# Kernel optimization log

Hardware: AMD Instinct MI355X
Metric: run time of the kernel (lower is better)

Reference implementation:

```python
import jax, jax.numpy as jnp
import numpy as np

B, S, D, H = 4, 2048, 512, 8
DEPTH = D // H


def setup_inputs() -> dict:
    key = jax.random.key(0)
    ks = jax.random.split(key, 12)
    s = 0.02
    return {
        "q": jax.random.normal(ks[0], (B, S, D), jnp.float32),
        "k": jax.random.normal(ks[1], (B, S, D), jnp.float32),
        "v": jax.random.normal(ks[2], (B, S, D), jnp.float32),
        "mask": jax.random.randint(ks[3], (B, 1, 1, S), 0, 2, jnp.int32),
        "wq": jax.random.normal(ks[4], (D, D), jnp.float32) * s,
        "bq": jnp.zeros((D,), jnp.float32),
        "wk": jax.random.normal(ks[5], (D, D), jnp.float32) * s,
        "bk": jnp.zeros((D,), jnp.float32),
        "wv": jax.random.normal(ks[6], (D, D), jnp.float32) * s,
        "bv": jnp.zeros((D,), jnp.float32),
        "wo": jax.random.normal(ks[7], (D, D), jnp.float32) * s,
        "bo": jnp.zeros((D,), jnp.float32),
    }


def _split_heads(x):
    # [B,S,D] -> [B,H,S,depth]
    b = x.shape[0]
    return x.reshape(b, -1, H, DEPTH).transpose(0, 2, 1, 3)


def reference(q, k, v, mask, wq, bq, wk, bk, wv, bv, wo, bo):
    qh = _split_heads(q @ wq + bq)
    kh = _split_heads(k @ wk + bk)
    vh = _split_heads(v @ wv + bv)
    scale = 1.0 / jnp.sqrt(jnp.float32(DEPTH))
    logits = jnp.einsum("bhqd,bhkd->bhqk", qh, kh) * scale
    logits = logits + mask.astype(jnp.float32) * -1e9
    attn = jax.nn.softmax(logits, axis=-1)  # [B,H,Sq,Sk]
    out = jnp.einsum("bhqk,bhkd->bhqd", attn, vh)
    out = out.transpose(0, 2, 1, 3).reshape(q.shape[0], -1, D)
    out = out @ wo + bo
    return out, attn
```

## Files before the change

### kernel.cpp

```cpp
#include <hip/hip_runtime.h>

#define B_ 4
#define S_ 2048
#define D_ 512
#define H_ 8
#define DP_ 64
#define NT_ (S_/64)

typedef __attribute__((ext_vector_type(4))) float f32x4;
typedef __attribute__((ext_vector_type(8))) short short8;
typedef __attribute__((ext_vector_type(4))) int i32x4;

__device__ __forceinline__ short f2bf(float f){
  unsigned u = __float_as_uint(f);
  u += 0x7fff + ((u >> 16) & 1);
  return (short)(u >> 16);
}

__device__ __forceinline__ int cvtpk(float lo, float hi){
  int r;
  asm("v_cvt_pk_bf16_f32 %0, %1, %2" : "=v"(r) : "v"(lo), "v"(hi));
  return r;
}

#define SWZ(r, kb) ((r)*64 + ((kb) ^ (((r)&7)<<3)))
#define F2(r) ((((r)&3)) | ((((r)>>3)&1)<<2))
#define SWZ2(r, kb) ((r)*64 + ((kb) ^ (F2(r)<<3)))

#define WAITV(N) do{ asm volatile("s_waitcnt vmcnt(" #N ")" ::: "memory"); }while(0)
#define BAR() do{ __builtin_amdgcn_s_barrier(); __builtin_amdgcn_sched_barrier(0); }while(0)

template<int NC>
__device__ __forceinline__ void stage_swz(const short* __restrict__ g, int rowStride,
                                          short* shbase, int w, int l){
  #pragma unroll
  for(int i = 0; i < NC; ++i){
    int byte = (w*NC + i)*1024 + l*16;
    int row = byte >> 7;
    int gs = ((byte >> 4) & 7) ^ (row & 7);
    const short* src = g + (size_t)row*rowStride + gs*8;
    __builtin_amdgcn_global_load_lds((const __attribute__((address_space(1))) void*)src,
        (__attribute__((address_space(3))) void*)(shbase + (w*NC + i)*512), 16, 0, 0);
  }
}
template<int NC>
__device__ __forceinline__ void stage_swz2(const short* __restrict__ g, int rowStride,
                                           short* shbase, int w, int l){
  #pragma unroll
  for(int i = 0; i < NC; ++i){
    int byte = (w*NC + i)*1024 + l*16;
    int row = byte >> 7;
    int gs = ((byte >> 4) & 7) ^ F2(row);
    const short* src = g + (size_t)row*rowStride + gs*8;
    __builtin_amdgcn_global_load_lds((const __attribute__((address_space(1))) void*)src,
        (__attribute__((address_space(3))) void*)(shbase + (w*NC + i)*512), 16, 0, 0);
  }
}

__global__ __launch_bounds__(256) void k_pre(const float* __restrict__ q,
        const float* __restrict__ k, const float* __restrict__ v,
        const int* __restrict__ mask,
        const float* __restrict__ w0, const float* __restrict__ w1,
        const float* __restrict__ w2, const float* __restrict__ w3,
        short* __restrict__ wT, short* __restrict__ qkvc, float* __restrict__ mb){
  __shared__ float tt[32][33];
  const int bi = blockIdx.x, t = threadIdx.x;
  if(bi < 1024){
    const int z = bi >> 8;
    const float* w = z == 0 ? w0 : z == 1 ? w1 : z == 2 ? w2 : w3;
    short* wt = wT + z * 262144;
    const int bxy = bi & 255;
    const int bx = (bxy & 15) * 32, by = (bxy >> 4) * 32;
    const int tx = t & 31, ty = t >> 5;
    #pragma unroll
    for(int i = 0; i < 32; i += 8) tt[ty + i][tx] = w[(by + ty + i) * D_ + bx + tx];
    __syncthreads();
    #pragma unroll
    for(int i = 0; i < 32; i += 8) wt[(bx + ty + i) * D_ + by + tx] = f2bf(tt[tx][ty + i]);
  } else if(bi < 7168){
    const int ci = bi - 1024;
    const int z = ci >> 11;
    const float* s = z == 0 ? q : z == 1 ? k : v;
    short* d = qkvc + (size_t)z * (B_ * S_ * D_);
    int i = (ci & 2047) * 256 + t;
    float4 a = ((const float4*)s)[i * 2];
    float4 b = ((const float4*)s)[i * 2 + 1];
    short8 o;
    o[0]=f2bf(a.x); o[1]=f2bf(a.y); o[2]=f2bf(a.z); o[3]=f2bf(a.w);
    o[4]=f2bf(b.x); o[5]=f2bf(b.y); o[6]=f2bf(b.z); o[7]=f2bf(b.w);
    ((short8*)d)[i] = o;
  } else {
    int i = (bi - 7168) * 256 + t;
    mb[i] = mask[i] ? -1.0e9f : 0.0f;
  }
}

__global__ __launch_bounds__(256) void k_gemm_qkv(const short* __restrict__ Xall,
        const short* __restrict__ WTall, const float* __restrict__ b0,
        const float* __restrict__ b1, const float* __restrict__ b2,
        short* __restrict__ qh, short* __restrict__ kh, short* __restrict__ vvt){
  __shared__ __align__(16) short As[8192];
  __shared__ __align__(16) short Bs[8192];
  const int z = blockIdx.z;
  const short* X  = Xall + (size_t)z * (B_*S_*D_);
  const short* WT = WTall + (size_t)z * (D_*D_);
  const float* bias = z==0 ? b0 : (z==1 ? b1 : b2);
  const int t = threadIdx.x, l = t & 63, w = t >> 6;
  const int lr = l & 15, lg = l >> 4;
  const int m0 = blockIdx.x * 128, n0 = blockIdx.y * 128;
  const int wr = w >> 1, wc = w & 1;
  const short* Xb = X + (size_t)m0 * D_;
  const short* Wb = WT + (size_t)n0 * D_;
  f32x4 acc[4][4] = {};
  for(int kt = 0; kt < D_ / 64; ++kt){
    stage_swz<4>(Xb + kt*64, D_, As, w, l);
    stage_swz<4>(Wb + kt*64, D_, Bs, w, l);
    __syncthreads();
    #pragma unroll
    for(int ks = 0; ks < 2; ++ks){
      const int kb = ks*32 + lg*8;
      short8 a[4], b[4];
      #pragma unroll
      for(int mt = 0; mt < 4; ++mt)
        a[mt] = *reinterpret_cast<const short8*>(&As[SWZ(wr*64 + mt*16 + lr, kb)]);
      #pragma unroll
      for(int nt = 0; nt < 4; ++nt)
        b[nt] = *reinterpret_cast<const short8*>(&Bs[SWZ(wc*64 + nt*16 + lr, kb)]);
      __builtin_amdgcn_s_setprio(1);
      #pragma unroll
      for(int mt = 0; mt < 4; ++mt)
        #pragma unroll
        for(int nt = 0; nt < 4; ++nt)
          acc[mt][nt] = __builtin_amdgcn_mfma_f32_16x16x32_bf16(a[mt], b[nt], acc[mt][nt], 0, 0, 0);
      __builtin_amdgcn_s_setprio(0);
    }
    __syncthreads();
  }
  #pragma unroll
  for(int mt = 0; mt < 4; ++mt){
    #pragma unroll
    for(int nt = 0; nt < 4; ++nt){
      const int n = n0 + wc*64 + nt*16 + lr;
      const int m4 = m0 + wr*64 + mt*16 + lg*4;
      float vals[4];
      #pragma unroll
      for(int r = 0; r < 4; ++r) vals[r] = acc[mt][nt][r] + bias[n];
      if(z == 2){
        short4 pv4;
        pv4.x = f2bf(vals[0]); pv4.y = f2bf(vals[1]); pv4.z = f2bf(vals[2]); pv4.w = f2bf(vals[3]);
        *reinterpret_cast<short4*>(&vvt[
            (((size_t)((m4 >> 11) * H_ + (n >> 6))) * DP_ + (n & 63)) * S_ + (m4 & 2047)]) = pv4;
      } else {
        short* dst = z == 0 ? qh : kh;
        #pragma unroll
        for(int r = 0; r < 4; ++r){
          int m = m4 + r;
          dst[(((size_t)((m >> 11) * H_ + (n >> 6))) * S_ + (m & 2047)) * DP_ + (n & 63)] = f2bf(vals[r]);
        }
      }
    }
  }
}

__global__ __launch_bounds__(256) void k_gemm_out(const short* __restrict__ X,
        const short* __restrict__ WT, const float* __restrict__ bias,
        float* __restrict__ Out){
  __shared__ __align__(16) short As[8192];
  __shared__ __align__(16) short Bs[8192];
  const int t = threadIdx.x, l = t & 63, w = t >> 6;
  const int lr = l & 15, lg = l >> 4;
  const int m0 = blockIdx.x * 128, n0 = blockIdx.y * 128;
  const int wr = w >> 1, wc = w & 1;
  const short* Xb = X + (size_t)m0 * D_;
  const short* Wb = WT + (size_t)n0 * D_;
  f32x4 acc[4][4] = {};
  for(int kt = 0; kt < D_ / 64; ++kt){
    stage_swz<4>(Xb + kt*64, D_, As, w, l);
    stage_swz<4>(Wb + kt*64, D_, Bs, w, l);
    __syncthreads();
    #pragma unroll
    for(int ks = 0; ks < 2; ++ks){
      const int kb = ks*32 + lg*8;
      short8 a[4], b[4];
      #pragma unroll
      for(int mt = 0; mt < 4; ++mt)
        a[mt] = *reinterpret_cast<const short8*>(&As[SWZ(wr*64 + mt*16 + lr, kb)]);
      #pragma unroll
      for(int nt = 0; nt < 4; ++nt)
        b[nt] = *reinterpret_cast<const short8*>(&Bs[SWZ(wc*64 + nt*16 + lr, kb)]);
      __builtin_amdgcn_s_setprio(1);
      #pragma unroll
      for(int mt = 0; mt < 4; ++mt)
        #pragma unroll
        for(int nt = 0; nt < 4; ++nt)
          acc[mt][nt] = __builtin_amdgcn_mfma_f32_16x16x32_bf16(a[mt], b[nt], acc[mt][nt], 0, 0, 0);
      __builtin_amdgcn_s_setprio(0);
    }
    __syncthreads();
  }
  #pragma unroll
  for(int mt = 0; mt < 4; ++mt){
    #pragma unroll
    for(int nt = 0; nt < 4; ++nt){
      const int n = n0 + wc*64 + nt*16 + lr;
      const int m4 = m0 + wr*64 + mt*16 + lg*4;
      #pragma unroll
      for(int r = 0; r < 4; ++r)
        Out[(size_t)(m4 + r) * D_ + n] = acc[mt][nt][r] + bias[n];
    }
  }
}

__global__ __launch_bounds__(512, 4) void k_attn(const short* __restrict__ qh,
                                                 const short* __restrict__ kh,
                                                 const short* __restrict__ vt,
                                                 const float* __restrict__ mb,
                                                 float* __restrict__ attn,
                                                 short* __restrict__ ctx){
  __shared__ __align__(16) short Sh[28672];
  const int t = threadIdx.x, l = t & 63, w = t >> 6;
  const int lr = l & 15, lg = l >> 4;
  int lin = blockIdx.y * 16 + blockIdx.x;
  int sw = (lin & 7) * 64 + (lin >> 3);
  const int bh = sw >> 4, b = bh >> 3, h = bh & 7;
  const int q0 = (sw & 15) * 128;
  const short* Qb = qh + (size_t)bh * S_ * DP_ + (size_t)q0 * DP_;
  const short* Kb = kh + (size_t)bh * S_ * DP_;
  const short* Vtb = vt + (size_t)bh * DP_ * S_;
  const float* Mbb = mb + b * S_;
  float* Mlds = (float*)(Sh + 24576);
  const float scale = 0.125f;

  stage_swz2<2>(Qb, DP_, Sh + 16384, w, l);
  __builtin_amdgcn_global_load_lds(
      (const __attribute__((address_space(1))) void*)(Mbb + w*256 + l*4),
      (__attribute__((address_space(3))) void*)(Mlds + w*256 + l*4), 16, 0, 0);
  stage_swz2<1>(Kb, DP_, Sh, w, l);
  stage_swz2<1>(Kb + 4096, DP_, Sh + 4096, w, l);
  stage_swz2<1>(Kb + 8192, DP_, Sh + 8192, w, l);
  WAITV(3); BAR();
  short8 bq0, bq1;
  {
    int r = w * 16 + lr;
    bq0 = *reinterpret_cast<const short8*>(&Sh[16384 + SWZ2(r, lg * 8)]);
    bq1 = *reinterpret_cast<const short8*>(&Sh[16384 + SWZ2(r, 32 + lg * 8)]);
  }

  float ps = 0.f;
  for(int kt = 0; kt < NT_; ++kt){
    if(kt <= NT_ - 3){ WAITV(2); } else if(kt == NT_ - 2){ WAITV(1); } else { WAITV(0); }
    BAR();
    if(kt + 3 < NT_)
      stage_swz2<1>(Kb + (size_t)(kt + 3) * 4096, DP_, Sh + ((kt + 3) & 3) * 4096, w, l);
    const short* Kc = Sh + (kt & 3) * 4096;
    const float* Ml = Mlds + kt * 64;
    #pragma unroll
    for(int st = 0; st < 4; ++st){
      const float4 mv = *(const float4*)&Ml[st * 16 + lg * 4];
      short8 ak0 = *reinterpret_cast<const short8*>(&Kc[SWZ2(st * 16 + lr, lg * 8)]);
      short8 ak1 = *reinterpret_cast<const short8*>(&Kc[SWZ2(st * 16 + lr, 32 + lg * 8)]);
      __builtin_amdgcn_s_setprio(1);
      f32x4 c = {};
      c = __builtin_amdgcn_mfma_f32_16x16x32_bf16(ak0, bq0, c, 0, 0, 0);
      c = __builtin_amdgcn_mfma_f32_16x16x32_bf16(ak1, bq1, c, 0, 0, 0);
      __builtin_amdgcn_s_setprio(0);
      ps += __expf(__builtin_fmaf(c[0], scale, mv.x));
      ps += __expf(__builtin_fmaf(c[1], scale, mv.y));
      ps += __expf(__builtin_fmaf(c[2], scale, mv.z));
      ps += __expf(__builtin_fmaf(c[3], scale, mv.w));
    }
  }
  BAR();
  stage_swz2<1>(Kb, DP_, Sh, w, l);
  stage_swz2<1>(Vtb, S_, Sh + 12288, w, l);
  stage_swz2<1>(Kb + 4096, DP_, Sh + 4096, w, l);
  stage_swz2<1>(Vtb + 64, S_, Sh + 16384, w, l);
  ps += __shfl_xor(ps, 16, 64);
  ps += __shfl_xor(ps, 32, 64);
  const float rinv = 1.f / ps;

  f32x4 o[4] = {};
  const int grow = ((lr >> 2) << 3) + (lr & 3);
  for(int kt = 0; kt < NT_; ++kt){
    if(kt == 0){ WAITV(2); }
    else if(kt == 1){ WAITV(6); }
    else if(kt == NT_ - 1){ WAITV(8); }
    else { WAITV(10); }
    BAR();
    if(kt + 2 < NT_){
      stage_swz2<1>(Kb + (size_t)(kt + 2) * 4096, DP_, Sh + ((kt + 2) % 3) * 4096, w, l);
      stage_swz2<1>(Vtb + (size_t)(kt + 2) * 64, S_, Sh + 12288 + ((kt + 2) % 3) * 4096, w, l);
    }
    const short* Kc = Sh + (kt % 3) * 4096;
    const short* Vc = Sh + 12288 + (kt % 3) * 4096;
    const float* Ml = Mlds + kt * 64;
    const int q = q0 + w * 16 + lr;
    i32x4 pav[2];
    #pragma unroll
    for(int st = 0; st < 4; ++st){
      const int ks = st >> 1, h4 = st & 1;
      const int row = grow + h4 * 4 + ks * 32;
      const int mcol = ks * 32 + h4 * 4 + lg * 8;
      const float4 mv = *(const float4*)&Ml[mcol];
      short8 ak0 = *reinterpret_cast<const short8*>(&Kc[SWZ2(row, lg * 8)]);
      short8 ak1 = *reinterpret_cast<const short8*>(&Kc[SWZ2(row, 32 + lg * 8)]);
      __builtin_amdgcn_s_setprio(1);
      f32x4 c = {};
      c = __builtin_amdgcn_mfma_f32_16x16x32_bf16(ak0, bq0, c, 0, 0, 0);
      c = __builtin_amdgcn_mfma_f32_16x16x32_bf16(ak1, bq1, c, 0, 0, 0);
      __builtin_amdgcn_s_setprio(0);
      float4 pw;
      pw.x = __expf(__builtin_fmaf(c[0], scale, mv.x)) * rinv;
      pw.y = __expf(__builtin_fmaf(c[1], scale, mv.y)) * rinv;
      pw.z = __expf(__builtin_fmaf(c[2], scale, mv.z)) * rinv;
      pw.w = __expf(__builtin_fmaf(c[3], scale, mv.w)) * rinv;
      *reinterpret_cast<float4*>(&attn[((size_t)bh * S_ + q) * S_ + kt * 64 + mcol]) = pw;
      pav[ks][h4 * 2 + 0] = cvtpk(pw.x, pw.y);
      pav[ks][h4 * 2 + 1] = cvtpk(pw.z, pw.w);
    }
    #pragma unroll
    for(int ks = 0; ks < 2; ++ks){
      short8 pa = __builtin_bit_cast(short8, pav[ks]);
      __builtin_amdgcn_s_setprio(1);
      #pragma unroll
      for(int dt = 0; dt < 4; ++dt){
        short8 vb = *reinterpret_cast<const short8*>(&Vc[SWZ2(dt * 16 + lr, ks * 32 + lg * 8)]);
        o[dt] = __builtin_amdgcn_mfma_f32_16x16x32_bf16(pa, vb, o[dt], 0, 0, 0);
      }
      __builtin_amdgcn_s_setprio(0);
    }
  }
  #pragma unroll
  for(int dt = 0; dt < 4; ++dt){
    #pragma unroll
    for(int r = 0; r < 4; ++r){
      int q = q0 + w * 16 + lg * 4 + r;
      int dd = h * 64 + dt * 16 + lr;
      ctx[((size_t)b * S_ + q) * D_ + dd] = f2bf(o[dt][r]);
    }
  }
}

extern "C" void kernel_launch(void* const* d_in, const int* in_sizes, int n_in,
                              void* d_out, int out_size, void* d_ws, size_t ws_size,
                              hipStream_t stream){
  const float* q  = (const float*)d_in[0];
  const float* k  = (const float*)d_in[1];
  const float* v  = (const float*)d_in[2];
  const int* mask = (const int*)d_in[3];
  const float* wq = (const float*)d_in[4];
  const float* bq = (const float*)d_in[5];
  const float* wk = (const float*)d_in[6];
  const float* bk = (const float*)d_in[7];
  const float* wv = (const float*)d_in[8];
  const float* bv = (const float*)d_in[9];
  const float* wo = (const float*)d_in[10];
  const float* bo = (const float*)d_in[11];

  float* out  = (float*)d_out;
  float* attn = out + (size_t)B_ * S_ * D_;

  char* ws = (char*)d_ws;
  short* qkvc = (short*)ws;
  short* qh  = (short*)(ws + 25165824);
  short* kh  = (short*)(ws + 33554432);
  short* vvt = (short*)(ws + 41943040);
  short* ctx = (short*)(ws + 50331648);
  short* wT  = (short*)(ws + 58720256);
  float* mb  = (float*)(ws + 58720256 + 4 * 524288);

  hipLaunchKernelGGL(k_pre, dim3(7200), dim3(256), 0, stream,
                     q, k, v, mask, wq, wk, wv, wo, wT, qkvc, mb);

  hipLaunchKernelGGL(k_gemm_qkv, dim3(64, 4, 3), dim3(256), 0, stream,
                     qkvc, wT, bq, bk, bv, qh, kh, vvt);

  hipLaunchKernelGGL(k_attn, dim3(16, 32), dim3(512), 0, stream, qh, kh, vvt, mb, attn, ctx);

  hipLaunchKernelGGL(k_gemm_out, dim3(64, 4), dim3(256), 0, stream, ctx, wT + 3 * 262144, bo, out);
}
```

Baseline: 244.4 us.

## Fuse fp32-to-bf16 input conversion into QKV GEMM and stream attn nontemporally

Removes the separate pass that converted q/k/v to bf16 in a workspace buffer. The QKV GEMM now loads fp32 activations directly, packs them to bf16 in registers and writes them into swizzled LDS. This avoids writing and re-reading roughly 24 MB of intermediate data, but gives up the async global_load_lds path for the A operand and reads twice as many bytes per tile. Separately, the large attention-probability output is now written with nontemporal stores so it does not pollute the cache.

```diff
diff --git a/kernel.cpp b/kernel.cpp
--- a/kernel.cpp
+++ b/kernel.cpp
@@ -57,12 +57,10 @@
   }
 }
 
-__global__ __launch_bounds__(256) void k_pre(const float* __restrict__ q,
-        const float* __restrict__ k, const float* __restrict__ v,
-        const int* __restrict__ mask,
+__global__ __launch_bounds__(256) void k_pre(const int* __restrict__ mask,
         const float* __restrict__ w0, const float* __restrict__ w1,
         const float* __restrict__ w2, const float* __restrict__ w3,
-        short* __restrict__ wT, short* __restrict__ qkvc, float* __restrict__ mb){
+        short* __restrict__ wT, float* __restrict__ mb){
   __shared__ float tt[32][33];
   const int bi = blockIdx.x, t = threadIdx.x;
   if(bi < 1024){
@@ -77,43 +75,43 @@
     __syncthreads();
     #pragma unroll
     for(int i = 0; i < 32; i += 8) wt[(bx + ty + i) * D_ + by + tx] = f2bf(tt[tx][ty + i]);
-  } else if(bi < 7168){
-    const int ci = bi - 1024;
-    const int z = ci >> 11;
-    const float* s = z == 0 ? q : z == 1 ? k : v;
-    short* d = qkvc + (size_t)z * (B_ * S_ * D_);
-    int i = (ci & 2047) * 256 + t;
-    float4 a = ((const float4*)s)[i * 2];
-    float4 b = ((const float4*)s)[i * 2 + 1];
-    short8 o;
-    o[0]=f2bf(a.x); o[1]=f2bf(a.y); o[2]=f2bf(a.z); o[3]=f2bf(a.w);
-    o[4]=f2bf(b.x); o[5]=f2bf(b.y); o[6]=f2bf(b.z); o[7]=f2bf(b.w);
-    ((short8*)d)[i] = o;
   } else {
-    int i = (bi - 7168) * 256 + t;
+    int i = (bi - 1024) * 256 + t;
     mb[i] = mask[i] ? -1.0e9f : 0.0f;
   }
 }
 
-__global__ __launch_bounds__(256) void k_gemm_qkv(const short* __restrict__ Xall,
+__global__ __launch_bounds__(256) void k_gemm_qkv(const float* __restrict__ qf,
+        const float* __restrict__ kf, const float* __restrict__ vf,
         const short* __restrict__ WTall, const float* __restrict__ b0,
         const float* __restrict__ b1, const float* __restrict__ b2,
         short* __restrict__ qh, short* __restrict__ kh, short* __restrict__ vvt){
   __shared__ __align__(16) short As[8192];
   __shared__ __align__(16) short Bs[8192];
   const int z = blockIdx.z;
-  const short* X  = Xall + (size_t)z * (B_*S_*D_);
+  const float* X = z == 0 ? qf : (z == 1 ? kf : vf);
   const short* WT = WTall + (size_t)z * (D_*D_);
   const float* bias = z==0 ? b0 : (z==1 ? b1 : b2);
   const int t = threadIdx.x, l = t & 63, w = t >> 6;
   const int lr = l & 15, lg = l >> 4;
   const int m0 = blockIdx.x * 128, n0 = blockIdx.y * 128;
   const int wr = w >> 1, wc = w & 1;
-  const short* Xb = X + (size_t)m0 * D_;
+  const float* Xb = X + (size_t)m0 * D_;
   const short* Wb = WT + (size_t)n0 * D_;
   f32x4 acc[4][4] = {};
   for(int kt = 0; kt < D_ / 64; ++kt){
-    stage_swz<4>(Xb + kt*64, D_, As, w, l);
+    #pragma unroll
+    for(int i = 0; i < 4; ++i){
+      int e = t + 256 * i;
+      int row = e >> 3, c8 = (e & 7) * 8;
+      const float* src = Xb + (size_t)row * D_ + kt * 64 + c8;
+      float4 f0 = *reinterpret_cast<const float4*>(src);
+      float4 f1 = *reinterpret_cast<const float4*>(src + 4);
+      i32x4 pk;
+      pk[0] = cvtpk(f0.x, f0.y); pk[1] = cvtpk(f0.z, f0.w);
+      pk[2] = cvtpk(f1.x, f1.y); pk[3] = cvtpk(f1.z, f1.w);
+      *reinterpret_cast<i32x4*>(&As[SWZ(row, c8)]) = pk;
+    }
     stage_swz<4>(Wb + kt*64, D_, Bs, w, l);
     __syncthreads();
     #pragma unroll
@@ -309,14 +307,15 @@
       c = __builtin_amdgcn_mfma_f32_16x16x32_bf16(ak0, bq0, c, 0, 0, 0);
       c = __builtin_amdgcn_mfma_f32_16x16x32_bf16(ak1, bq1, c, 0, 0, 0);
       __builtin_amdgcn_s_setprio(0);
-      float4 pw;
-      pw.x = __expf(__builtin_fmaf(c[0], scale, mv.x)) * rinv;
-      pw.y = __expf(__builtin_fmaf(c[1], scale, mv.y)) * rinv;
-      pw.z = __expf(__builtin_fmaf(c[2], scale, mv.z)) * rinv;
-      pw.w = __expf(__builtin_fmaf(c[3], scale, mv.w)) * rinv;
-      *reinterpret_cast<float4*>(&attn[((size_t)bh * S_ + q) * S_ + kt * 64 + mcol]) = pw;
-      pav[ks][h4 * 2 + 0] = cvtpk(pw.x, pw.y);
-      pav[ks][h4 * 2 + 1] = cvtpk(pw.z, pw.w);
+      f32x4 pw;
+      pw[0] = __expf(__builtin_fmaf(c[0], scale, mv.x)) * rinv;
+      pw[1] = __expf(__builtin_fmaf(c[1], scale, mv.y)) * rinv;
+      pw[2] = __expf(__builtin_fmaf(c[2], scale, mv.z)) * rinv;
+      pw[3] = __expf(__builtin_fmaf(c[3], scale, mv.w)) * rinv;
+      __builtin_nontemporal_store(pw,
+          reinterpret_cast<f32x4*>(&attn[((size_t)bh * S_ + q) * S_ + kt * 64 + mcol]));
+      pav[ks][h4 * 2 + 0] = cvtpk(pw[0], pw[1]);
+      pav[ks][h4 * 2 + 1] = cvtpk(pw[2], pw[3]);
     }
     #pragma unroll
     for(int ks = 0; ks < 2; ++ks){
@@ -361,19 +360,18 @@
   float* attn = out + (size_t)B_ * S_ * D_;
 
   char* ws = (char*)d_ws;
-  short* qkvc = (short*)ws;
-  short* qh  = (short*)(ws + 25165824);
-  short* kh  = (short*)(ws + 33554432);
-  short* vvt = (short*)(ws + 41943040);
-  short* ctx = (short*)(ws + 50331648);
-  short* wT  = (short*)(ws + 58720256);
-  float* mb  = (float*)(ws + 58720256 + 4 * 524288);
-
-  hipLaunchKernelGGL(k_pre, dim3(7200), dim3(256), 0, stream,
-                     q, k, v, mask, wq, wk, wv, wo, wT, qkvc, mb);
+  short* qh  = (short*)(ws);
+  short* kh  = (short*)(ws + 8388608);
+  short* vvt = (short*)(ws + 16777216);
+  short* ctx = (short*)(ws + 25165824);
+  short* wT  = (short*)(ws + 33554432);
+  float* mb  = (float*)(ws + 33554432 + 4 * 524288);
+
+  hipLaunchKernelGGL(k_pre, dim3(1056), dim3(256), 0, stream,
+                     mask, wq, wk, wv, wo, wT, mb);
 
   hipLaunchKernelGGL(k_gemm_qkv, dim3(64, 4, 3), dim3(256), 0, stream,
-                     qkvc, wT, bq, bk, bv, qh, kh, vvt);
+                     q, k, v, wT, bq, bk, bv, qh, kh, vvt);
 
   hipLaunchKernelGGL(k_attn, dim3(16, 32), dim3(512), 0, stream, qh, kh, vvt, mb, attn, ctx);
 
```

After: 414.0 us. 1.69x slower.
